# Performance work log

Measured on AMD Instinct MI355X. Metric: run time of the kernel, lower is better.

Reference implementation:

```python
import jax, jax.numpy as jnp
import numpy as np

EPS = 1e-8  # torch CosineSimilarity default eps

B, T, D, K = 16, 1024, 2048, 64


def setup_inputs() -> dict:
    key = jax.random.key(0)
    k1, k2, k3 = jax.random.split(key, 3)
    inputs = jax.random.normal(k1, (B, T, D), dtype=jnp.float32)
    class_avgs = jax.random.normal(k2, (K, D), dtype=jnp.float32)
    labels = jax.random.randint(k3, (B, T), 0, K, dtype=jnp.int64)
    return {"inputs": inputs, "class_avgs": class_avgs, "labels": labels}


def _simrel_forward(inputs, class_avgs, labels):
    # inputs: [B, T, D]; class_avgs: [K, D]; labels: [B, T] int
    # Faithful training-mode forward: sequential running-mean prototype
    # update per token (row-major over batch then sequence), cosine sims
    # computed against the prototype state *before* each token's update.
    b, t, d = inputs.shape
    k = class_avgs.shape[0]
    vecs = inputs.reshape(b * t, d)
    labs = labels.reshape(b * t)
    class_ids = jnp.arange(k)

    def step(carry, xs):
        avgs, counts = carry          # [K, D], [K]
        vec, label = xs               # [D], scalar int
        nv = jnp.maximum(jnp.sqrt(jnp.sum(vec * vec)), EPS)
        na = jnp.maximum(jnp.sqrt(jnp.sum(avgs * avgs, axis=1)), EPS)  # [K]
        cos = (avgs @ vec) / (na * nv)                                 # [K]
        is_inf = jnp.any(jnp.isinf(avgs), axis=1)                      # [K]
        self_sim = jnp.sum(vec * vec) / (nv * nv)  # cosine(vec, vec)
        is_label = class_ids == label
        sims = jnp.where(is_inf, jnp.where(is_label, self_sim, -1.0), cos)
        # running-mean update of the labeled class prototype
        c = counts[label]
        old = avgs[label]
        new_row = jnp.where(is_inf[label], vec, (old * c + vec) / (c + 1.0))
        avgs = avgs.at[label].set(new_row)
        counts = counts.at[label].add(1.0)
        return (avgs, counts), sims

    counts0 = jnp.zeros((k,), dtype=inputs.dtype)
    (_, _), sims = jax.lax.scan(step, (class_avgs, counts0), (vecs, labs))
    return sims.reshape(b, t, k)


def reference(inputs, class_avgs, labels):
    return _simrel_forward(inputs, class_avgs, labels)
```

## Files before the change

### kernel.cpp

```cpp
#include <hip/hip_runtime.h>
#include <hip/hip_bf16.h>

#define N_TOK 16384
#define DIM 2048
#define KCLS 64
#define JRANGES 32
#define RANGE 512
#define KC 64
#define EPS 1e-8f

typedef short bf16x8 __attribute__((ext_vector_type(8)));
typedef unsigned short u16x8 __attribute__((ext_vector_type(8)));
typedef float f32x4 __attribute__((ext_vector_type(4)));

__device__ __forceinline__ unsigned short f2bf(float f) {
    unsigned u = __float_as_uint(f);
    u += 0x7fffu + ((u >> 16) & 1u);
    return (unsigned short)(u >> 16);
}
__device__ __forceinline__ float bf2f(unsigned short s) {
    return __uint_as_float(((unsigned)s) << 16);
}

__device__ __forceinline__ float dpp_sum64(float x) {
    x += __int_as_float(__builtin_amdgcn_update_dpp(0, __float_as_int(x), 0x111, 0xf, 0xf, true));
    x += __int_as_float(__builtin_amdgcn_update_dpp(0, __float_as_int(x), 0x112, 0xf, 0xf, true));
    x += __int_as_float(__builtin_amdgcn_update_dpp(0, __float_as_int(x), 0x114, 0xf, 0xf, true));
    x += __int_as_float(__builtin_amdgcn_update_dpp(0, __float_as_int(x), 0x118, 0xf, 0xf, true));
    x += __int_as_float(__builtin_amdgcn_update_dpp(0, __float_as_int(x), 0x142, 0xf, 0xf, true));
    x += __int_as_float(__builtin_amdgcn_update_dpp(0, __float_as_int(x), 0x143, 0xf, 0xf, true));
    return x;
}

__global__ __launch_bounds__(256) void fix_labels_kernel(
    const int* __restrict__ raw, int* __restrict__ lab) {
    __shared__ int not64;
    int t = threadIdx.x, b = blockIdx.x;
    if (t == 0) not64 = 0;
    __syncthreads();
    int n0 = b * 256 + t;
    int lo = raw[2 * n0], hi = raw[2 * n0 + 1];
    if (hi != 0 || lo < 0 || lo >= KCLS) atomicOr(&not64, 1);
    __syncthreads();
    lab[n0] = not64 ? raw[n0] : raw[2 * n0];
}

__global__ __launch_bounds__(256) void prep_kernel(
    const float* __restrict__ x, unsigned short* __restrict__ xb,
    float* __restrict__ vnorm2) {
    int w4 = threadIdx.x >> 6, lane = threadIdx.x & 63;
    int n = blockIdx.x * 4 + w4;
    const float* v = x + (size_t)n * DIM;
    unsigned short* o = xb + (size_t)n * DIM;
    float p = 0.f;
#pragma unroll
    for (int it = 0; it < 8; it++) {
        float4 a = *(const float4*)(v + it * 256 + lane * 4);
        p = fmaf(a.x, a.x, p); p = fmaf(a.y, a.y, p);
        p = fmaf(a.z, a.z, p); p = fmaf(a.w, a.w, p);
        ushort4 h = make_ushort4(f2bf(a.x), f2bf(a.y), f2bf(a.z), f2bf(a.w));
        *(ushort4*)(o + it * 256 + lane * 4) = h;
    }
    p = dpp_sum64(p);
    if (lane == 63) vnorm2[n] = p;
}

__global__ __launch_bounds__(256) void partials_kernel(
    const unsigned short* __restrict__ xb, const int* __restrict__ lab,
    float* __restrict__ spart, int* __restrict__ cnt_range) {
    int bid = blockIdx.x;
    int j = bid & 31, k = bid >> 5;
    int t = threadIdx.x;
    __shared__ int ll[RANGE];
    __shared__ short ml[RANGE];
    __shared__ int nm_s;
    for (int i = t; i < RANGE; i += 256) ll[i] = lab[j * RANGE + i];
    __syncthreads();
    if (t == 0) {
        int nm = 0;
        for (int i = 0; i < RANGE; i++)
            if (ll[i] == k) ml[nm++] = (short)i;
        nm_s = nm;
        cnt_range[j * KCLS + k] = nm;
    }
    __syncthreads();
    int nm = nm_s;
    float acc[8] = {0, 0, 0, 0, 0, 0, 0, 0};
    for (int m = 0; m < nm; m++) {
        const unsigned short* r = xb + (size_t)(j * RANGE + (int)ml[m]) * DIM + t * 8;
        u16x8 hv = *(const u16x8*)r;
#pragma unroll
        for (int i = 0; i < 8; i++) acc[i] += bf2f(hv[i]);
    }
    float* dst = spart + ((size_t)j * KCLS + k) * DIM + t * 8;
    *(float4*)dst = make_float4(acc[0], acc[1], acc[2], acc[3]);
    *(float4*)(dst + 4) = make_float4(acc[4], acc[5], acc[6], acc[7]);
}

__global__ __launch_bounds__(256) void scan_kernel(
    const float* __restrict__ avgs, float* __restrict__ spart,
    unsigned short* __restrict__ Sb,
    const int* __restrict__ cnt_range, int* __restrict__ cnt_before) {
    int t = blockIdx.x * 256 + threadIdx.x;
    int k = t >> 9;
    int d4 = t & 511;
    int d = d4 * 4;
    float4 run = {0, 0, 0, 0};
    int cb = 0;
    float4 init = *(const float4*)(avgs + (size_t)k * DIM + d);
    for (int j = 0; j < JRANGES; j++) {
        size_t idx = ((size_t)j * KCLS + k) * DIM + d;
        float4 part = *(const float4*)(spart + idx);
        float4 w = (cb == 0) ? init : run;
        *(float4*)(spart + idx) = w;
        *(ushort4*)(Sb + idx) = make_ushort4(f2bf(w.x), f2bf(w.y), f2bf(w.z), f2bf(w.w));
        if (d4 == 0) cnt_before[j * KCLS + k] = cb;
        run.x += part.x; run.y += part.y; run.z += part.z; run.w += part.w;
        cb += cnt_range[j * KCLS + k];
    }
}

__global__ __launch_bounds__(64) void snapnorm_kernel(
    const float* __restrict__ spart, float* __restrict__ n2snap) {
    int b = blockIdx.x;
    int lane = threadIdx.x;
    const float* row = spart + (size_t)b * DIM;
    float s = 0.f;
#pragma unroll
    for (int i = 0; i < 8; i++) {
        float4 v = *(const float4*)(row + i * 256 + lane * 4);
        s = fmaf(v.x, v.x, s); s = fmaf(v.y, v.y, s);
        s = fmaf(v.z, v.z, s); s = fmaf(v.w, v.w, s);
    }
    s = dpp_sum64(s);
    if (lane == 63) n2snap[b] = s;
}

__device__ __forceinline__ void stage_panel(
    const unsigned short* __restrict__ src, short* dst, int nunits,
    int t, int kcoff) {
#pragma unroll
    for (int i = 0; i < 2; i++) {
        int u = t + 512 * i;
        if (u < nunits) {
            int row = u >> 3, gsw = u & 7;
            int g = gsw ^ (row & 7);
            const unsigned short* s = src + (size_t)row * DIM + kcoff + g * 8;
            __builtin_amdgcn_global_load_lds(
                (__attribute__((address_space(1))) void*)s,
                (__attribute__((address_space(3))) void*)(dst + u * 8),
                16, 0, 0);
        }
    }
}

__global__ __launch_bounds__(512, 4) void gemm_kernel(
    const unsigned short* __restrict__ xb, const unsigned short* __restrict__ Sb,
    float* __restrict__ D0, unsigned short* __restrict__ Gbf) {
    __shared__ short PI[2][128 * KC];
    __shared__ short PJ[2][128 * KC];
    static const char TIa[14] = {0,1,1,2,2,2,3,3,3,3, 0,1,2,3};
    static const char TJa[14] = {0,0,1,0,1,2,0,1,2,3, 0,0,0,0};

    int bid = blockIdx.x;
    int j = bid & 31;
    int tt = bid >> 5;
    int I = TIa[tt], J = TJa[tt];
    bool isD = (tt >= 10);
    bool diag = (!isD) && (I == J);
    int start = j * RANGE;
    int t = threadIdx.x, lane = t & 63, w = t >> 6;
    int rw = w & 3, cw = w >> 2;
    int NCF = isD ? 2 : 4;
    int colbase = isD ? cw * 32 : cw * 64;

    f32x4 acc[2][4];
#pragma unroll
    for (int a = 0; a < 2; a++)
#pragma unroll
        for (int b = 0; b < 4; b++) acc[a][b] = (f32x4){0.f, 0.f, 0.f, 0.f};

    const unsigned short* srcI = xb + (size_t)(start + I * 128) * DIM;
    const unsigned short* srcJ = isD ? (Sb + (size_t)(j * KCLS) * DIM)
                                     : (xb + (size_t)(start + J * 128) * DIM);
    int nJu = isD ? 512 : 1024;

    stage_panel(srcI, PI[0], 1024, t, 0);
    if (!diag) stage_panel(srcJ, PJ[0], nJu, t, 0);
    __syncthreads();

    for (int kc = 0; kc < DIM / KC; kc++) {
        int cur = kc & 1;
        if (kc + 1 < DIM / KC) {
            stage_panel(srcI, PI[cur ^ 1], 1024, t, (kc + 1) * KC);
            if (!diag) stage_panel(srcJ, PJ[cur ^ 1], nJu, t, (kc + 1) * KC);
        }
        const short* PA = PI[cur];
        const short* PB = diag ? PI[cur] : PJ[cur];
#pragma unroll
        for (int kk = 0; kk < 2; kk++) {
            int kb = kk * 32 + (lane >> 4) * 8;
            int ra = rw * 32 + (lane & 15);
            bf16x8 a0 = *(const bf16x8*)&PA[ra * KC + (kb ^ ((ra & 7) << 3))];
            int ra1 = ra + 16;
            bf16x8 a1 = *(const bf16x8*)&PA[ra1 * KC + (kb ^ ((ra1 & 7) << 3))];
#pragma unroll
            for (int f = 0; f < 4; f++) {
                if (f < NCF) {
                    int rb = colbase + f * 16 + (lane & 15);
                    bf16x8 bb = *(const bf16x8*)&PB[rb * KC + (kb ^ ((rb & 7) << 3))];
                    acc[0][f] = __builtin_amdgcn_mfma_f32_16x16x32_bf16(a0, bb, acc[0][f], 0, 0, 0);
                    acc[1][f] = __builtin_amdgcn_mfma_f32_16x16x32_bf16(a1, bb, acc[1][f], 0, 0, 0);
                }
            }
        }
        __syncthreads();
    }

    if (!isD) {
        size_t gbase = (size_t)j * (512 * 512);
#pragma unroll
        for (int rf = 0; rf < 2; rf++)
#pragma unroll
            for (int f = 0; f < 4; f++)
#pragma unroll
                for (int r = 0; r < 4; r++) {
                    int lrow = I * 128 + rw * 32 + rf * 16 + (lane >> 4) * 4 + r;
                    int lcol = J * 128 + colbase + f * 16 + (lane & 15);
                    unsigned short hv = f2bf(acc[rf][f][r]);
                    Gbf[gbase + (size_t)lrow * 512 + lcol] = hv;
                    if (I != J)
                        Gbf[gbase + (size_t)lcol * 512 + lrow] = hv;
                }
    } else {
#pragma unroll
        for (int rf = 0; rf < 2; rf++)
#pragma unroll
            for (int f = 0; f < 2; f++)
#pragma unroll
                for (int r = 0; r < 4; r++) {
                    int grow = start + I * 128 + rw * 32 + rf * 16 + (lane >> 4) * 4 + r;
                    int gcol = colbase + f * 16 + (lane & 15);
                    D0[(size_t)grow * KCLS + gcol] = acc[rf][f][r];
                }
    }
}

__global__ __launch_bounds__(512) void finalize_kernel(
    const int* __restrict__ lab, const float* __restrict__ D0,
    const unsigned short* __restrict__ Gbf, const float* __restrict__ vnorm2,
    const float* __restrict__ n2snap, const int* __restrict__ cnt_before,
    float* __restrict__ out) {
    __shared__ unsigned char lbl[RANGE];
    __shared__ short evl[RANGE];
    __shared__ short evcnt_s[8];
    __shared__ short evoff_s[9];
    __shared__ float corrb[8][RANGE];
    __shared__ float cntb[8][RANGE];
    __shared__ float rdv[RANGE];
    __shared__ float invna[RANGE + 8];
    __shared__ unsigned char vgs[8];

    int bid = blockIdx.x;
    int g = bid >> 5, jr = bid & 31;
    int g8 = g * 8;
    int start = jr * RANGE;
    int t = threadIdx.x, lane = t & 63, w = t >> 6;
    int c = g8 + w;

    lbl[t] = (unsigned char)lab[start + t];
    if (t < 8) vgs[t] = (cnt_before[jr * KCLS + g8 + t] == 0) ? 1 : 0;
    __syncthreads();

    unsigned char myl[8];
    int cntL = 0;
#pragma unroll
    for (int i = 0; i < 8; i++) {
        myl[i] = lbl[lane * 8 + i];
        cntL += (myl[i] == c) ? 1 : 0;
    }
    int pre = cntL;
    for (int s = 1; s < 64; s <<= 1) {
        int v = __shfl_up(pre, s, 64);
        if (lane >= s) pre += v;
    }
    int tot = __shfl(pre, 63, 64);
    if (lane == 63) evcnt_s[w] = (short)tot;
    __syncthreads();
    if (t == 0) {
        int s = 0;
        for (int i = 0; i < 8; i++) { evoff_s[i] = (short)s; s += evcnt_s[i]; }
        evoff_s[8] = (short)s;
    }
    __syncthreads();
    int off = evoff_s[w], m = evcnt_s[w];
    {
        int wr = off + (pre - cntL);
#pragma unroll
        for (int i = 0; i < 8; i++)
            if (myl[i] == c) evl[wr++] = (short)(lane * 8 + i);
    }
    __syncthreads();

    const unsigned short* grb = Gbf + (size_t)jr * 262144;
    int vg = vgs[w];
#pragma unroll 1
    for (int chk = 0; chk < 8; chk++) {
        int tk = chk * 64 + lane;
        float corr = 0.f;
        int cnt = 0;
#pragma unroll 1
        for (int i = 0; i < m; i++) {
            int e = evl[off + i];
            float gv = bf2f(grb[(size_t)e * 512 + tk]);
            bool after = (tk > e);
            corr += after ? gv : 0.f;
            cnt += after ? 1 : 0;
        }
        corrb[w][tk] = corr;
        cntb[w][tk] = (float)cnt;
        if ((int)lbl[tk] == c) {
            float d0v = vg ? 0.f : D0[(size_t)(start + tk) * KCLS + c];
            rdv[off + cnt] = d0v + corr;
        }
    }
    __syncthreads();

    if (t < 8) {
        int o = evoff_s[t], mm = evcnt_s[t];
        int vgt = vgs[t];
        float n2 = n2snap[jr * KCLS + g8 + t];
        invna[o + t] = 1.0f / fmaxf(sqrtf(n2), EPS);
        for (int i = 1; i <= mm; i++) {
            int e = evl[o + i - 1];
            float xn2 = vnorm2[start + e];
            if (vgt && i == 1) n2 = xn2;
            else n2 += 2.f * rdv[o + i - 1] + xn2;
            invna[o + t + i] = 1.0f / fmaxf(sqrtf(n2), EPS);
        }
    }
    __syncthreads();

    {
        float4 d0a = *(const float4*)&D0[(size_t)(start + t) * KCLS + g8];
        float4 d0b = *(const float4*)&D0[(size_t)(start + t) * KCLS + g8 + 4];
        float d0[8] = {d0a.x, d0a.y, d0a.z, d0a.w, d0b.x, d0b.y, d0b.z, d0b.w};
        float nvinv = 1.0f / fmaxf(sqrtf(vnorm2[start + t]), EPS);
        float o8[8];
#pragma unroll
        for (int cc = 0; cc < 8; cc++) {
            float corr = corrb[cc][t];
            int cnt = (int)cntb[cc][t];
            float dot = (vgs[cc] && cnt > 0) ? corr : (d0[cc] + corr);
            o8[cc] = dot * invna[evoff_s[cc] + cc + cnt] * nvinv;
        }
        float4 oa = {o8[0], o8[1], o8[2], o8[3]};
        float4 ob = {o8[4], o8[5], o8[6], o8[7]};
        float* op = &out[(size_t)(start + t) * KCLS + g8];
        *(float4*)op = oa;
        *(float4*)(op + 4) = ob;
    }
}

extern "C" void kernel_launch(void* const* d_in, const int* in_sizes, int n_in,
                              void* d_out, int out_size, void* d_ws, size_t ws_size,
                              hipStream_t stream) {
    const float* inputs = (const float*)d_in[0];
    const float* class_avgs = (const float*)d_in[1];
    const int* labels_raw = (const int*)d_in[2];
    float* out = (float*)d_out;
    char* ws = (char*)d_ws;

    size_t off = 0;
    int* lab = (int*)(ws + off);          off += (size_t)N_TOK * 4;
    int* cnt_range = (int*)(ws + off);    off += (size_t)JRANGES * KCLS * 4;
    int* cnt_before = (int*)(ws + off);   off += (size_t)JRANGES * KCLS * 4;
    float* n2snap = (float*)(ws + off);   off += (size_t)JRANGES * KCLS * 4;
    float* vnorm2 = (float*)(ws + off);   off += (size_t)N_TOK * 4;
    off = (off + 255) & ~(size_t)255;
    unsigned short* Xb = (unsigned short*)(ws + off);
    off += (size_t)N_TOK * DIM * 2;
    unsigned short* Sb = (unsigned short*)(ws + off);
    off += (size_t)JRANGES * KCLS * DIM * 2;
    float* D0 = (float*)(ws + off);       off += (size_t)N_TOK * KCLS * 4;
    float* spart = (float*)(ws + off);
    unsigned short* Gbf = (unsigned short*)spart;

    fix_labels_kernel<<<N_TOK / 256, 256, 0, stream>>>(labels_raw, lab);
    prep_kernel<<<N_TOK / 4, 256, 0, stream>>>(inputs, Xb, vnorm2);
    partials_kernel<<<JRANGES * KCLS, 256, 0, stream>>>(Xb, lab, spart, cnt_range);
    scan_kernel<<<(KCLS * (DIM / 4)) / 256, 256, 0, stream>>>(class_avgs, spart, Sb,
                                                              cnt_range, cnt_before);
    snapnorm_kernel<<<JRANGES * KCLS, 64, 0, stream>>>(spart, n2snap);
    gemm_kernel<<<14 * JRANGES, 512, 0, stream>>>(Xb, Sb, D0, Gbf);
    finalize_kernel<<<8 * JRANGES, 512, 0, stream>>>(lab, D0, Gbf, vnorm2, n2snap,
                                                     cnt_before, out);
}
```

Before: 186.5 us.

## Fuse label fix and snapshot norms into neighbors; stage transposed Gram tile via LDS

Folds the label-normalisation kernel into the prep kernel, which now also zeroes n2snap. Snapshot squared norms are computed inside the scan kernel with a wave reduction and atomicAdd, so the separate snapnorm kernel is dropped. The mirrored half of each Gram tile is written through a swizzled LDS buffer so it goes out as coalesced 16-byte stores instead of strided 2-byte scatter. This removes two launches and an extra read of spart, at the cost of float atomics with nondeterministic summation order and an extra barrier in the GEMM epilogue.

```diff
diff --git a/kernel.cpp b/kernel.cpp
--- a/kernel.cpp
+++ b/kernel.cpp
@@ -32,24 +32,25 @@
     return x;
 }
 
-__global__ __launch_bounds__(256) void fix_labels_kernel(
-    const int* __restrict__ raw, int* __restrict__ lab) {
-    __shared__ int not64;
-    int t = threadIdx.x, b = blockIdx.x;
-    if (t == 0) not64 = 0;
-    __syncthreads();
-    int n0 = b * 256 + t;
-    int lo = raw[2 * n0], hi = raw[2 * n0 + 1];
-    if (hi != 0 || lo < 0 || lo >= KCLS) atomicOr(&not64, 1);
-    __syncthreads();
-    lab[n0] = not64 ? raw[n0] : raw[2 * n0];
-}
-
 __global__ __launch_bounds__(256) void prep_kernel(
     const float* __restrict__ x, unsigned short* __restrict__ xb,
-    float* __restrict__ vnorm2) {
-    int w4 = threadIdx.x >> 6, lane = threadIdx.x & 63;
-    int n = blockIdx.x * 4 + w4;
+    float* __restrict__ vnorm2, const int* __restrict__ raw,
+    int* __restrict__ lab, float* __restrict__ n2snap) {
+    int bid = blockIdx.x, tid = threadIdx.x;
+    if (bid < 64) {
+        __shared__ int not64;
+        if (tid == 0) not64 = 0;
+        __syncthreads();
+        int n0 = bid * 256 + tid;
+        int lo = raw[2 * n0], hi = raw[2 * n0 + 1];
+        if (hi != 0 || lo < 0 || lo >= KCLS) atomicOr(&not64, 1);
+        __syncthreads();
+        lab[n0] = not64 ? raw[n0] : raw[2 * n0];
+    } else if (bid < 72) {
+        n2snap[(bid - 64) * 256 + tid] = 0.f;
+    }
+    int w4 = tid >> 6, lane = tid & 63;
+    int n = bid * 4 + w4;
     const float* v = x + (size_t)n * DIM;
     unsigned short* o = xb + (size_t)n * DIM;
     float p = 0.f;
@@ -99,9 +100,10 @@
 
 __global__ __launch_bounds__(256) void scan_kernel(
     const float* __restrict__ avgs, float* __restrict__ spart,
-    unsigned short* __restrict__ Sb,
+    unsigned short* __restrict__ Sb, float* __restrict__ n2snap,
     const int* __restrict__ cnt_range, int* __restrict__ cnt_before) {
     int t = blockIdx.x * 256 + threadIdx.x;
+    int lane = threadIdx.x & 63;
     int k = t >> 9;
     int d4 = t & 511;
     int d = d4 * 4;
@@ -114,26 +116,15 @@
         float4 w = (cb == 0) ? init : run;
         *(float4*)(spart + idx) = w;
         *(ushort4*)(Sb + idx) = make_ushort4(f2bf(w.x), f2bf(w.y), f2bf(w.z), f2bf(w.w));
+        float s = 0.f;
+        s = fmaf(w.x, w.x, s); s = fmaf(w.y, w.y, s);
+        s = fmaf(w.z, w.z, s); s = fmaf(w.w, w.w, s);
+        s = dpp_sum64(s);
+        if (lane == 63) atomicAdd(&n2snap[j * KCLS + k], s);
         if (d4 == 0) cnt_before[j * KCLS + k] = cb;
         run.x += part.x; run.y += part.y; run.z += part.z; run.w += part.w;
         cb += cnt_range[j * KCLS + k];
     }
-}
-
-__global__ __launch_bounds__(64) void snapnorm_kernel(
-    const float* __restrict__ spart, float* __restrict__ n2snap) {
-    int b = blockIdx.x;
-    int lane = threadIdx.x;
-    const float* row = spart + (size_t)b * DIM;
-    float s = 0.f;
-#pragma unroll
-    for (int i = 0; i < 8; i++) {
-        float4 v = *(const float4*)(row + i * 256 + lane * 4);
-        s = fmaf(v.x, v.x, s); s = fmaf(v.y, v.y, s);
-        s = fmaf(v.z, v.z, s); s = fmaf(v.w, v.w, s);
-    }
-    s = dpp_sum64(s);
-    if (lane == 63) n2snap[b] = s;
 }
 
 __device__ __forceinline__ void stage_panel(
@@ -219,19 +210,30 @@
 
     if (!isD) {
         size_t gbase = (size_t)j * (512 * 512);
+        short* TT = &PI[0][0];
 #pragma unroll
         for (int rf = 0; rf < 2; rf++)
 #pragma unroll
             for (int f = 0; f < 4; f++)
 #pragma unroll
                 for (int r = 0; r < 4; r++) {
-                    int lrow = I * 128 + rw * 32 + rf * 16 + (lane >> 4) * 4 + r;
-                    int lcol = J * 128 + colbase + f * 16 + (lane & 15);
+                    int lr = rw * 32 + rf * 16 + (lane >> 4) * 4 + r;
+                    int lc = colbase + f * 16 + (lane & 15);
                     unsigned short hv = f2bf(acc[rf][f][r]);
-                    Gbf[gbase + (size_t)lrow * 512 + lcol] = hv;
+                    Gbf[gbase + (size_t)(I * 128 + lr) * 512 + J * 128 + lc] = hv;
                     if (I != J)
-                        Gbf[gbase + (size_t)lcol * 512 + lrow] = hv;
+                        TT[lc * 128 + (lr ^ ((lc & 15) << 3))] = (short)hv;
                 }
+        if (I != J) {
+            __syncthreads();
+#pragma unroll
+            for (int i = 0; i < 4; i++) {
+                int u = t + 512 * i;
+                int tr = u >> 4, tc = u & 15;
+                u16x8 v = *(const u16x8*)&TT[tr * 128 + ((tc * 8) ^ ((tr & 15) << 3))];
+                *(u16x8*)&Gbf[gbase + (size_t)(J * 128 + tr) * 512 + I * 128 + tc * 8] = v;
+            }
+        }
     } else {
 #pragma unroll
         for (int rf = 0; rf < 2; rf++)
@@ -386,12 +388,12 @@
     float* spart = (float*)(ws + off);
     unsigned short* Gbf = (unsigned short*)spart;
 
-    fix_labels_kernel<<<N_TOK / 256, 256, 0, stream>>>(labels_raw, lab);
-    prep_kernel<<<N_TOK / 4, 256, 0, stream>>>(inputs, Xb, vnorm2);
+    prep_kernel<<<N_TOK / 4, 256, 0, stream>>>(inputs, Xb, vnorm2, labels_raw,
+                                               lab, n2snap);
     partials_kernel<<<JRANGES * KCLS, 256, 0, stream>>>(Xb, lab, spart, cnt_range);
     scan_kernel<<<(KCLS * (DIM / 4)) / 256, 256, 0, stream>>>(class_avgs, spart, Sb,
-                                                              cnt_range, cnt_before);
-    snapnorm_kernel<<<JRANGES * KCLS, 64, 0, stream>>>(spart, n2snap);
+                                                              n2snap, cnt_range,
+                                                              cnt_before);
     gemm_kernel<<<14 * JRANGES, 512, 0, stream>>>(Xb, Sb, D0, Gbf);
     finalize_kernel<<<8 * JRANGES, 512, 0, stream>>>(lab, D0, Gbf, vnorm2, n2snap,
                                                      cnt_before, out);
```

Measured after the change: 179.5 us. -3.7%, faster.
